# Kernel tuning notes

Hardware: AMD Instinct MI355X
Metric: run time of the kernel (lower is better)

Reference implementation:

```python
import jax, jax.numpy as jnp
import numpy as np

N, M, D = 1024, 1024, 256

def setup_inputs() -> dict:
    key = jax.random.key(0)
    ks = jax.random.split(key, 10)
    s = 1.0 / np.sqrt(D)
    return {
        "f_r": jax.random.normal(ks[0], (N, D), jnp.float32),
        "f_r_prime": jax.random.normal(ks[1], (M, D), jnp.float32),
        "W_w": jax.random.uniform(ks[2], (D, D), jnp.float32, -s, s),
        "W_b": jax.random.uniform(ks[3], (D,), jnp.float32, -s, s),
        "Wp_w": jax.random.uniform(ks[4], (D, D), jnp.float32, -s, s),
        "Wp_b": jax.random.uniform(ks[5], (D,), jnp.float32, -s, s),
        "w_w": jax.random.uniform(ks[6], (1, D), jnp.float32, -s, s),
        "w_b": jax.random.uniform(ks[7], (1,), jnp.float32, -s, s),
        "wp_w": jax.random.uniform(ks[8], (1, D), jnp.float32, -s, s),
        "wp_b": jax.random.uniform(ks[9], (1,), jnp.float32, -s, s),
    }

def reference(f_r, f_r_prime, W_w, W_b, Wp_w, Wp_b, w_w, w_b, wp_w, wp_b):
    q = f_r @ W_w.T + W_b            # [N, D]
    k = f_r_prime @ Wp_w.T + Wp_b    # [M, D]
    # additive (Bahdanau) scores: tanh over broadcast sum [N, M, D]
    h = jnp.tanh(q[:, None, :] + k[None, :, :])
    alpha = h @ w_w.T + w_b          # [N, M, 1]
    alpha = jax.nn.softmax(alpha, axis=1)
    # stage-1 pooling over M (weights on raw f_r_prime, as in source)
    context = jnp.sum(alpha * f_r_prime[None, :, :], axis=1)  # [N, D]
    # stage-2 attention pooling over N
    alpha_p = jax.nn.softmax(context @ wp_w.T + wp_b, axis=0)  # [N, 1]
    pool = jnp.sum(alpha_p * context, axis=0, keepdims=True)   # [1, D]
    return pool
```

## Files before the change

### kernel.cpp

```cpp
#include <hip/hip_runtime.h>

#define NN 1024
#define MM 1024
#define DD 256

__device__ __forceinline__ float rcp_fast(float x) { return __builtin_amdgcn_rcpf(x); }

__global__ __launch_bounds__(256) void gemm_exp_kernel(
    const float* __restrict__ f_r,  const float* __restrict__ W_w,  const float* __restrict__ W_b,
    const float* __restrict__ f_rp, const float* __restrict__ Wp_w, const float* __restrict__ Wp_b,
    float* __restrict__ Eq, float* __restrict__ EkT, float* __restrict__ out0)
{
    const int b    = blockIdx.x;
    const int mat  = b >> 7;
    const int tile = b & 127;
    const int rt = tile & 31, dt = tile >> 5;
    const float* __restrict__ A    = mat ? f_rp : f_r;
    const float* __restrict__ B    = mat ? Wp_w : W_w;
    const float* __restrict__ bias = mat ? Wp_b : W_b;

    __shared__ float As[32][36];
    __shared__ float Bs[32][68];
    __shared__ float T[64][36];

    const int t  = threadIdx.x;
    if (b == 0) out0[t] = 0.f;
    const int tx = t & 15, ty = t >> 4;
    const int r0 = rt * 32, d0 = dt * 64;
    const int ar = t >> 3, ak = (t & 7) * 4;
    const int br = t >> 2, bk = (t & 3) * 8;

    float acc[2][4];
    #pragma unroll
    for (int i = 0; i < 2; ++i)
        #pragma unroll
        for (int j = 0; j < 4; ++j) acc[i][j] = 0.f;

    for (int kk = 0; kk < DD; kk += 32) {
        float4 av  = *(const float4*)(A + (size_t)(r0 + ar) * DD + kk + ak);
        float4 bv0 = *(const float4*)(B + (size_t)(d0 + br) * DD + kk + bk);
        float4 bv1 = *(const float4*)(B + (size_t)(d0 + br) * DD + kk + bk + 4);
        __syncthreads();
        As[ak + 0][ar] = av.x; As[ak + 1][ar] = av.y; As[ak + 2][ar] = av.z; As[ak + 3][ar] = av.w;
        Bs[bk + 0][br] = bv0.x; Bs[bk + 1][br] = bv0.y; Bs[bk + 2][br] = bv0.z; Bs[bk + 3][br] = bv0.w;
        Bs[bk + 4][br] = bv1.x; Bs[bk + 5][br] = bv1.y; Bs[bk + 6][br] = bv1.z; Bs[bk + 7][br] = bv1.w;
        __syncthreads();
        #pragma unroll
        for (int k = 0; k < 32; ++k) {
            float2 a2 = *(const float2*)&As[k][ty * 2];
            float4 b4 = *(const float4*)&Bs[k][tx * 4];
            float aa[2] = {a2.x, a2.y};
            float bb[4] = {b4.x, b4.y, b4.z, b4.w};
            #pragma unroll
            for (int i = 0; i < 2; ++i)
                #pragma unroll
                for (int j = 0; j < 4; ++j)
                    acc[i][j] = fmaf(aa[i], bb[j], acc[i][j]);
        }
    }

    float bj[4];
    #pragma unroll
    for (int j = 0; j < 4; ++j) bj[j] = bias[d0 + tx * 4 + j];

    float e[2][4];
    #pragma unroll
    for (int i = 0; i < 2; ++i)
        #pragma unroll
        for (int j = 0; j < 4; ++j) {
            float v = acc[i][j] + bj[j];
            v = fminf(fmaxf(v, -10.f), 10.f);
            e[i][j] = __expf(2.f * v);
        }

    if (mat == 0) {
        #pragma unroll
        for (int i = 0; i < 2; ++i)
            *(float4*)&Eq[(size_t)(r0 + ty * 2 + i) * DD + d0 + tx * 4] =
                make_float4(e[i][0], e[i][1], e[i][2], e[i][3]);
    } else {
        __syncthreads();
        #pragma unroll
        for (int i = 0; i < 2; ++i)
            #pragma unroll
            for (int j = 0; j < 4; ++j) T[tx * 4 + j][ty * 2 + i] = e[i][j];
        __syncthreads();
        const int dl = t >> 3, rl = (t & 7) * 4;
        #pragma unroll
        for (int h = 0; h < 2; ++h) {
            int dloc = dl + 32 * h;
            float4 tv = *(const float4*)&T[dloc][rl];
            *(float4*)&EkT[(size_t)(d0 + dloc) * MM + r0 + rl] = tv;
        }
    }
}

__global__ __launch_bounds__(512, 8) void score_softmax_kernel(
    const float* __restrict__ Eq, const float* __restrict__ EkT,
    const float* __restrict__ w_w, float* __restrict__ alpha)
{
    __shared__ float eq[2 * DD];
    __shared__ float w2[DD];
    __shared__ float accbuf[8][256];
    __shared__ float redmx[8 * 2];
    __shared__ float redsm[8 * 2];

    const int t  = threadIdx.x;
    const int tg = t >> 8;
    const int tm = t & 255;
    const int lane = t & 63, wid = t >> 6;
    const int n0 = blockIdx.x * 2;
    const int dh = tg * 128;

    eq[t] = Eq[(size_t)n0 * DD + t];
    if (t < DD) w2[t] = -2.0f * w_w[t];
    __syncthreads();

    float acc[2][4];
    #pragma unroll
    for (int n = 0; n < 2; ++n)
        #pragma unroll
        for (int j = 0; j < 4; ++j) acc[n][j] = 0.f;

    const float* ekb = EkT + (size_t)dh * MM + 4 * tm;

    for (int g = 0; g < 32; ++g) {
        const int db = g * 4;
        float4 k0 = *(const float4*)(ekb + (size_t)(db + 0) * MM);
        float4 k1 = *(const float4*)(ekb + (size_t)(db + 1) * MM);
        float4 k2 = *(const float4*)(ekb + (size_t)(db + 2) * MM);
        float4 k3 = *(const float4*)(ekb + (size_t)(db + 3) * MM);
        float4 w4 = *(const float4*)&w2[dh + db];
        float4 qA = *(const float4*)&eq[dh + db];
        float4 qB = *(const float4*)&eq[DD + dh + db];

        float ka[2][4] = {{k0.x, k0.y, k0.z, k0.w}, {k2.x, k2.y, k2.z, k2.w}};
        float kb[2][4] = {{k1.x, k1.y, k1.z, k1.w}, {k3.x, k3.y, k3.z, k3.w}};
        float wa[2] = {w4.x, w4.z}, wb[2] = {w4.y, w4.w};
        float qa[2][2] = {{qA.x, qA.z}, {qB.x, qB.z}};
        float qb[2][2] = {{qA.y, qA.w}, {qB.y, qB.w}};

        #pragma unroll
        for (int pp = 0; pp < 2; ++pp)
            #pragma unroll
            for (int n = 0; n < 2; ++n)
                #pragma unroll
                for (int j = 0; j < 4; ++j) {
                    float x0 = fmaf(qa[n][pp], ka[pp][j], 1.f);
                    float x1 = fmaf(qb[n][pp], kb[pp][j], 1.f);
                    float p  = x0 * x1;
                    float tn = fmaf(wb[pp], x0, wa[pp] * x1);
                    acc[n][j] = fmaf(tn, rcp_fast(p), acc[n][j]);
                }
    }

    if (tg == 1) {
        #pragma unroll
        for (int n = 0; n < 2; ++n)
            #pragma unroll
            for (int j = 0; j < 4; ++j) accbuf[n * 4 + j][tm] = acc[n][j];
    }
    __syncthreads();
    if (tg == 0) {
        #pragma unroll
        for (int n = 0; n < 2; ++n)
            #pragma unroll
            for (int j = 0; j < 4; ++j) acc[n][j] += accbuf[n * 4 + j][tm];
    }

    float mx[2];
    #pragma unroll
    for (int n = 0; n < 2; ++n) {
        mx[n] = (tg == 0) ? fmaxf(fmaxf(acc[n][0], acc[n][1]), fmaxf(acc[n][2], acc[n][3])) : -3e38f;
        #pragma unroll
        for (int off = 32; off > 0; off >>= 1) mx[n] = fmaxf(mx[n], __shfl_xor(mx[n], off));
    }
    if (lane == 0) { redmx[wid * 2] = mx[0]; redmx[wid * 2 + 1] = mx[1]; }
    __syncthreads();
    float MX[2];
    #pragma unroll
    for (int n = 0; n < 2; ++n) {
        float m = redmx[n];
        #pragma unroll
        for (int w = 1; w < 8; ++w) m = fmaxf(m, redmx[w * 2 + n]);
        MX[n] = m;
    }

    float e[2][4], sm[2];
    #pragma unroll
    for (int n = 0; n < 2; ++n) {
        sm[n] = 0.f;
        #pragma unroll
        for (int j = 0; j < 4; ++j) {
            e[n][j] = (tg == 0) ? __expf(acc[n][j] - MX[n]) : 0.f;
            sm[n] += e[n][j];
        }
        #pragma unroll
        for (int off = 32; off > 0; off >>= 1) sm[n] += __shfl_xor(sm[n], off);
    }
    if (lane == 0) { redsm[wid * 2] = sm[0]; redsm[wid * 2 + 1] = sm[1]; }
    __syncthreads();
    if (tg == 0) {
        #pragma unroll
        for (int n = 0; n < 2; ++n) {
            float s = redsm[n];
            #pragma unroll
            for (int w = 1; w < 8; ++w) s += redsm[w * 2 + n];
            float inv = rcp_fast(s);
            *(float4*)&alpha[(size_t)(n0 + n) * MM + 4 * tm] =
                make_float4(e[n][0] * inv, e[n][1] * inv, e[n][2] * inv, e[n][3] * inv);
        }
    }
}

__global__ __launch_bounds__(256) void context_kernel(
    const float* __restrict__ alpha, const float* __restrict__ frp,
    float* __restrict__ part)
{
    __shared__ float als[16][128];
    const int t  = threadIdx.x;
    const int bm = blockIdx.x & 7;
    const int bn = blockIdx.x >> 3;
    const int dq = t & 63;
    const int ng = t >> 6;

    #pragma unroll
    for (int i = 0; i < 2; ++i) {
        int f4i = t + i * 256;
        int row = f4i >> 5, c4 = f4i & 31;
        *(float4*)&als[row][c4 * 4] =
            *(const float4*)&alpha[(size_t)(bn * 16 + row) * MM + bm * 128 + c4 * 4];
    }
    __syncthreads();

    float acc[4][4];
    #pragma unroll
    for (int n = 0; n < 4; ++n)
        #pragma unroll
        for (int j = 0; j < 4; ++j) acc[n][j] = 0.f;

    const float* fb = frp + (size_t)(bm * 128) * DD + 4 * dq;
    for (int m4 = 0; m4 < 32; ++m4) {
        float av[4][4];
        #pragma unroll
        for (int n = 0; n < 4; ++n) {
            float4 a4 = *(const float4*)&als[ng * 4 + n][m4 * 4];
            av[n][0] = a4.x; av[n][1] = a4.y; av[n][2] = a4.z; av[n][3] = a4.w;
        }
        #pragma unroll
        for (int mm = 0; mm < 4; ++mm) {
            float4 f4 = *(const float4*)(fb + (size_t)(m4 * 4 + mm) * DD);
            float fv[4] = {f4.x, f4.y, f4.z, f4.w};
            #pragma unroll
            for (int n = 0; n < 4; ++n)
                #pragma unroll
                for (int j = 0; j < 4; ++j)
                    acc[n][j] = fmaf(av[n][mm], fv[j], acc[n][j]);
        }
    }
    #pragma unroll
    for (int n = 0; n < 4; ++n)
        *(float4*)&part[((size_t)bm << 18) + (size_t)(bn * 16 + ng * 4 + n) * DD + 4 * dq] =
            make_float4(acc[n][0], acc[n][1], acc[n][2], acc[n][3]);
}

__global__ __launch_bounds__(256) void ctx_reduce_kernel(
    const float* __restrict__ part, const float* __restrict__ wp_w,
    float* __restrict__ ctx, float* __restrict__ score)
{
    __shared__ float red[4];
    const int t = threadIdx.x;
    const int n = blockIdx.x;
    const int lane = t & 63, wid = t >> 6;
    size_t idx = (size_t)n * DD + t;
    float c = 0.f;
    #pragma unroll
    for (int s = 0; s < 8; ++s) c += part[idx + ((size_t)s << 18)];
    ctx[idx] = c;
    float p = c * wp_w[t];
    #pragma unroll
    for (int off = 32; off > 0; off >>= 1) p += __shfl_xor(p, off);
    if (lane == 0) red[wid] = p;
    __syncthreads();
    if (t == 0) score[n] = red[0] + red[1] + red[2] + red[3];
}

__global__ __launch_bounds__(256) void pool_kernel(
    const float* __restrict__ ctx, const float* __restrict__ score,
    float* __restrict__ out)
{
    __shared__ float red[8];
    __shared__ float wloc[16];
    const int t = threadIdx.x, lane = t & 63, wid = t >> 6;

    float s0 = score[t], s1 = score[t + 256], s2 = score[t + 512], s3 = score[t + 768];
    float mx = fmaxf(fmaxf(s0, s1), fmaxf(s2, s3));
    #pragma unroll
    for (int off = 32; off > 0; off >>= 1) mx = fmaxf(mx, __shfl_xor(mx, off));
    if (lane == 0) red[wid] = mx;
    __syncthreads();
    mx = fmaxf(fmaxf(red[0], red[1]), fmaxf(red[2], red[3]));

    float se = __expf(s0 - mx) + __expf(s1 - mx) + __expf(s2 - mx) + __expf(s3 - mx);
    #pragma unroll
    for (int off = 32; off > 0; off >>= 1) se += __shfl_xor(se, off);
    if (lane == 0) red[4 + wid] = se;
    __syncthreads();
    se = red[4] + red[5] + red[6] + red[7];
    float invS = rcp_fast(se);

    if (t < 16) wloc[t] = __expf(score[blockIdx.x * 16 + t] - mx) * invS;
    __syncthreads();

    float pool = 0.f;
    const float* cb = ctx + (size_t)(blockIdx.x * 16) * DD + t;
    #pragma unroll
    for (int i = 0; i < 16; ++i) pool = fmaf(wloc[i], cb[i * DD], pool);
    atomicAdd(out + t, pool);
}

extern "C" void kernel_launch(void* const* d_in, const int* in_sizes, int n_in,
                              void* d_out, int out_size, void* d_ws, size_t ws_size,
                              hipStream_t stream) {
    const float* f_r  = (const float*)d_in[0];
    const float* f_rp = (const float*)d_in[1];
    const float* W_w  = (const float*)d_in[2];
    const float* W_b  = (const float*)d_in[3];
    const float* Wp_w = (const float*)d_in[4];
    const float* Wp_b = (const float*)d_in[5];
    const float* w_w  = (const float*)d_in[6];
    const float* wp_w = (const float*)d_in[8];
    float* out = (float*)d_out;

    float* ws    = (float*)d_ws;
    float* Eq    = ws;
    float* EkT   = ws + 262144;
    float* alpha = ws + 524288;
    float* part  = ws + 1572864;
    float* ctx   = ws + 3670016;
    float* score = ws + 3932160;

    gemm_exp_kernel<<<256, 256, 0, stream>>>(f_r, W_w, W_b, f_rp, Wp_w, Wp_b, Eq, EkT, out);
    score_softmax_kernel<<<512, 512, 0, stream>>>(Eq, EkT, w_w, alpha);
    context_kernel<<<512, 256, 0, stream>>>(alpha, f_rp, part);
    ctx_reduce_kernel<<<1024, 256, 0, stream>>>(part, wp_w, ctx, score);
    pool_kernel<<<64, 256, 0, stream>>>(ctx, score, out);
}
```

Measured before the change: 135.3 us.

## Precompute stage-2 scores algebraically, fold context reduce into pool, pack score math

```diff
diff --git a/kernel.cpp b/kernel.cpp
--- a/kernel.cpp
+++ b/kernel.cpp
@@ -4,14 +4,41 @@
 #define MM 1024
 #define DD 256
 
+typedef float floatx2 __attribute__((ext_vector_type(2)));
+
 __device__ __forceinline__ float rcp_fast(float x) { return __builtin_amdgcn_rcpf(x); }
 
 __global__ __launch_bounds__(256) void gemm_exp_kernel(
     const float* __restrict__ f_r,  const float* __restrict__ W_w,  const float* __restrict__ W_b,
     const float* __restrict__ f_rp, const float* __restrict__ Wp_w, const float* __restrict__ Wp_b,
-    float* __restrict__ Eq, float* __restrict__ EkT, float* __restrict__ out0)
+    const float* __restrict__ wp_w,
+    float* __restrict__ Eq, float* __restrict__ EkT, float* __restrict__ g,
+    float* __restrict__ out0)
 {
-    const int b    = blockIdx.x;
+    __shared__ float As[32][36];
+    __shared__ float Bs[32][68];
+    __shared__ float T[64][36];
+
+    const int b = blockIdx.x;
+    const int t = threadIdx.x;
+
+    if (b >= 256) {
+        const int gb = b - 256;
+        if (gb == 0) out0[t] = 0.f;
+        const int m = gb * 256 + t;
+        const float4* fm = (const float4*)(f_rp + (size_t)m * DD);
+        const float4* wp = (const float4*)wp_w;
+        float a0 = 0.f, a1 = 0.f, a2 = 0.f, a3 = 0.f;
+        #pragma unroll 8
+        for (int j = 0; j < 64; ++j) {
+            float4 v = fm[j], w = wp[j];
+            a0 = fmaf(v.x, w.x, a0); a1 = fmaf(v.y, w.y, a1);
+            a2 = fmaf(v.z, w.z, a2); a3 = fmaf(v.w, w.w, a3);
+        }
+        g[m] = (a0 + a1) + (a2 + a3);
+        return;
+    }
+
     const int mat  = b >> 7;
     const int tile = b & 127;
     const int rt = tile & 31, dt = tile >> 5;
@@ -19,12 +46,6 @@
     const float* __restrict__ B    = mat ? Wp_w : W_w;
     const float* __restrict__ bias = mat ? Wp_b : W_b;
 
-    __shared__ float As[32][36];
-    __shared__ float Bs[32][68];
-    __shared__ float T[64][36];
-
-    const int t  = threadIdx.x;
-    if (b == 0) out0[t] = 0.f;
     const int tx = t & 15, ty = t >> 4;
     const int r0 = rt * 32, d0 = dt * 64;
     const int ar = t >> 3, ak = (t & 7) * 4;
@@ -69,7 +90,7 @@
         #pragma unroll
         for (int j = 0; j < 4; ++j) {
             float v = acc[i][j] + bj[j];
-            v = fminf(fmaxf(v, -10.f), 10.f);
+            v = fminf(fmaxf(v, -5.f), 5.f);
             e[i][j] = __expf(2.f * v);
         }
 
@@ -95,15 +116,17 @@
     }
 }
 
-__global__ __launch_bounds__(512, 8) void score_softmax_kernel(
+__global__ __launch_bounds__(512, 4) void score_softmax_kernel(
     const float* __restrict__ Eq, const float* __restrict__ EkT,
-    const float* __restrict__ w_w, float* __restrict__ alpha)
+    const float* __restrict__ w_w, const float* __restrict__ g,
+    float* __restrict__ alpha, float* __restrict__ score)
 {
     __shared__ float eq[2 * DD];
     __shared__ float w2[DD];
     __shared__ float accbuf[8][256];
     __shared__ float redmx[8 * 2];
     __shared__ float redsm[8 * 2];
+    __shared__ float redg[4 * 2];
 
     const int t  = threadIdx.x;
     const int tg = t >> 8;
@@ -116,42 +139,64 @@
     if (t < DD) w2[t] = -2.0f * w_w[t];
     __syncthreads();
 
-    float acc[2][4];
-    #pragma unroll
-    for (int n = 0; n < 2; ++n)
-        #pragma unroll
-        for (int j = 0; j < 4; ++j) acc[n][j] = 0.f;
+    const floatx2 one2 = {1.f, 1.f};
+    floatx2 accl[2] = {{0.f, 0.f}, {0.f, 0.f}};
+    floatx2 acch[2] = {{0.f, 0.f}, {0.f, 0.f}};
 
     const float* ekb = EkT + (size_t)dh * MM + 4 * tm;
 
-    for (int g = 0; g < 32; ++g) {
-        const int db = g * 4;
-        float4 k0 = *(const float4*)(ekb + (size_t)(db + 0) * MM);
-        float4 k1 = *(const float4*)(ekb + (size_t)(db + 1) * MM);
-        float4 k2 = *(const float4*)(ekb + (size_t)(db + 2) * MM);
-        float4 k3 = *(const float4*)(ekb + (size_t)(db + 3) * MM);
+    float4 c0 = *(const float4*)(ekb + 0 * MM);
+    float4 c1 = *(const float4*)(ekb + 1 * MM);
+    float4 c2 = *(const float4*)(ekb + 2 * MM);
+    float4 c3 = *(const float4*)(ekb + 3 * MM);
+
+    for (int gi = 0; gi < 32; ++gi) {
+        float4 p0 = c0, p1 = c1, p2 = c2, p3 = c3;
+        if (gi < 31) {
+            const float* nb = ekb + (size_t)(gi * 4 + 4) * MM;
+            p0 = *(const float4*)(nb + 0 * MM);
+            p1 = *(const float4*)(nb + 1 * MM);
+            p2 = *(const float4*)(nb + 2 * MM);
+            p3 = *(const float4*)(nb + 3 * MM);
+        }
+        const int db = gi * 4;
         float4 w4 = *(const float4*)&w2[dh + db];
         float4 qA = *(const float4*)&eq[dh + db];
         float4 qB = *(const float4*)&eq[DD + dh + db];
 
-        float ka[2][4] = {{k0.x, k0.y, k0.z, k0.w}, {k2.x, k2.y, k2.z, k2.w}};
-        float kb[2][4] = {{k1.x, k1.y, k1.z, k1.w}, {k3.x, k3.y, k3.z, k3.w}};
-        float wa[2] = {w4.x, w4.z}, wb[2] = {w4.y, w4.w};
-        float qa[2][2] = {{qA.x, qA.z}, {qB.x, qB.z}};
-        float qb[2][2] = {{qA.y, qA.w}, {qB.y, qB.w}};
-
-        #pragma unroll
-        for (int pp = 0; pp < 2; ++pp)
-            #pragma unroll
-            for (int n = 0; n < 2; ++n)
-                #pragma unroll
-                for (int j = 0; j < 4; ++j) {
-                    float x0 = fmaf(qa[n][pp], ka[pp][j], 1.f);
-                    float x1 = fmaf(qb[n][pp], kb[pp][j], 1.f);
-                    float p  = x0 * x1;
-                    float tn = fmaf(wb[pp], x0, wa[pp] * x1);
-                    acc[n][j] = fmaf(tn, rcp_fast(p), acc[n][j]);
-                }
+        floatx2 kv[4][2] = {{{c0.x, c0.y}, {c0.z, c0.w}},
+                            {{c1.x, c1.y}, {c1.z, c1.w}},
+                            {{c2.x, c2.y}, {c2.z, c2.w}},
+                            {{c3.x, c3.y}, {c3.z, c3.w}}};
+        float ws[4] = {w4.x, w4.y, w4.z, w4.w};
+        float qs[2][4] = {{qA.x, qA.y, qA.z, qA.w}, {qB.x, qB.y, qB.z, qB.w}};
+
+        #pragma unroll
+        for (int h = 0; h < 2; ++h) {
+            #pragma unroll
+            for (int n = 0; n < 2; ++n) {
+                floatx2 x0 = qs[n][0] * kv[0][h] + one2;
+                floatx2 x1 = qs[n][1] * kv[1][h] + one2;
+                floatx2 x2 = qs[n][2] * kv[2][h] + one2;
+                floatx2 x3 = qs[n][3] * kv[3][h] + one2;
+                floatx2 p01 = x0 * x1;
+                floatx2 p23 = x2 * x3;
+                floatx2 n01 = ws[0] * x1 + ws[1] * x0;
+                floatx2 n23 = ws[2] * x3 + ws[3] * x2;
+                floatx2 nc  = n01 * p23 + n23 * p01;
+                floatx2 pt  = p01 * p23;
+                floatx2 r;  r.x = rcp_fast(pt.x);  r.y = rcp_fast(pt.y);
+                if (h == 0) accl[n] += nc * r; else acch[n] += nc * r;
+            }
+        }
+        c0 = p0; c1 = p1; c2 = p2; c3 = p3;
+    }
+
+    float acc[2][4];
+    #pragma unroll
+    for (int n = 0; n < 2; ++n) {
+        acc[n][0] = accl[n].x; acc[n][1] = accl[n].y;
+        acc[n][2] = acch[n].x; acc[n][3] = acch[n].y;
     }
 
     if (tg == 1) {
@@ -201,16 +246,25 @@
     if (lane == 0) { redsm[wid * 2] = sm[0]; redsm[wid * 2 + 1] = sm[1]; }
     __syncthreads();
     if (tg == 0) {
+        float4 g4 = *(const float4*)&g[4 * tm];
+        float sn[2];
         #pragma unroll
         for (int n = 0; n < 2; ++n) {
             float s = redsm[n];
             #pragma unroll
             for (int w = 1; w < 8; ++w) s += redsm[w * 2 + n];
             float inv = rcp_fast(s);
-            *(float4*)&alpha[(size_t)(n0 + n) * MM + 4 * tm] =
-                make_float4(e[n][0] * inv, e[n][1] * inv, e[n][2] * inv, e[n][3] * inv);
-        }
-    }
+            float a0 = e[n][0] * inv, a1 = e[n][1] * inv, a2 = e[n][2] * inv, a3 = e[n][3] * inv;
+            *(float4*)&alpha[(size_t)(n0 + n) * MM + 4 * tm] = make_float4(a0, a1, a2, a3);
+            sn[n] = fmaf(a0, g4.x, fmaf(a1, g4.y, fmaf(a2, g4.z, a3 * g4.w)));
+            #pragma unroll
+            for (int off = 32; off > 0; off >>= 1) sn[n] += __shfl_xor(sn[n], off);
+        }
+        if (lane == 0) { redg[wid * 2] = sn[0]; redg[wid * 2 + 1] = sn[1]; }
+    }
+    __syncthreads();
+    if (t == 0) score[n0]     = redg[0] + redg[2] + redg[4] + redg[6];
+    if (t == 1) score[n0 + 1] = redg[1] + redg[3] + redg[5] + redg[7];
 }
 
 __global__ __launch_bounds__(256) void context_kernel(
@@ -264,34 +318,13 @@
             make_float4(acc[n][0], acc[n][1], acc[n][2], acc[n][3]);
 }
 
-__global__ __launch_bounds__(256) void ctx_reduce_kernel(
-    const float* __restrict__ part, const float* __restrict__ wp_w,
-    float* __restrict__ ctx, float* __restrict__ score)
-{
-    __shared__ float red[4];
-    const int t = threadIdx.x;
-    const int n = blockIdx.x;
-    const int lane = t & 63, wid = t >> 6;
-    size_t idx = (size_t)n * DD + t;
-    float c = 0.f;
-    #pragma unroll
-    for (int s = 0; s < 8; ++s) c += part[idx + ((size_t)s << 18)];
-    ctx[idx] = c;
-    float p = c * wp_w[t];
-    #pragma unroll
-    for (int off = 32; off > 0; off >>= 1) p += __shfl_xor(p, off);
-    if (lane == 0) red[wid] = p;
-    __syncthreads();
-    if (t == 0) score[n] = red[0] + red[1] + red[2] + red[3];
-}
-
 __global__ __launch_bounds__(256) void pool_kernel(
-    const float* __restrict__ ctx, const float* __restrict__ score,
+    const float* __restrict__ part, const float* __restrict__ score,
     float* __restrict__ out)
 {
     __shared__ float red[8];
-    __shared__ float wloc[16];
     const int t = threadIdx.x, lane = t & 63, wid = t >> 6;
+    const int n0 = blockIdx.x * 4;
 
     float s0 = score[t], s1 = score[t + 256], s2 = score[t + 512], s3 = score[t + 768];
     float mx = fmaxf(fmaxf(s0, s1), fmaxf(s2, s3));
@@ -309,14 +342,17 @@
     se = red[4] + red[5] + red[6] + red[7];
     float invS = rcp_fast(se);
 
-    if (t < 16) wloc[t] = __expf(score[blockIdx.x * 16 + t] - mx) * invS;
-    __syncthreads();
-
-    float pool = 0.f;
-    const float* cb = ctx + (size_t)(blockIdx.x * 16) * DD + t;
-    #pragma unroll
-    for (int i = 0; i < 16; ++i) pool = fmaf(wloc[i], cb[i * DD], pool);
-    atomicAdd(out + t, pool);
+    float r = 0.f;
+    #pragma unroll
+    for (int i = 0; i < 4; ++i) {
+        float ap = __expf(score[n0 + i] - mx) * invS;
+        size_t idx = (size_t)(n0 + i) * DD + t;
+        float c = 0.f;
+        #pragma unroll
+        for (int s = 0; s < 8; ++s) c += part[idx + ((size_t)s << 18)];
+        r = fmaf(ap, c, r);
+    }
+    atomicAdd(out + t, r);
 }
 
 extern "C" void kernel_launch(void* const* d_in, const int* in_sizes, int n_in,
@@ -337,12 +373,12 @@
     float* EkT   = ws + 262144;
     float* alpha = ws + 524288;
     float* part  = ws + 1572864;
-    float* ctx   = ws + 3670016;
-    float* score = ws + 3932160;
-
-    gemm_exp_kernel<<<256, 256, 0, stream>>>(f_r, W_w, W_b, f_rp, Wp_w, Wp_b, Eq, EkT, out);
-    score_softmax_kernel<<<512, 512, 0, stream>>>(Eq, EkT, w_w, alpha);
+    float* score = ws + 3670016;
+    float* g     = ws + 3671040;
+
+    gemm_exp_kernel<<<260, 256, 0, stream>>>(f_r, W_w, W_b, f_rp, Wp_w, Wp_b, wp_w,
+                                             Eq, EkT, g, out);
+    score_softmax_kernel<<<512, 512, 0, stream>>>(Eq, EkT, w_w, g, alpha, score);
     context_kernel<<<512, 256, 0, stream>>>(alpha, f_rp, part);
-    ctx_reduce_kernel<<<1024, 256, 0, stream>>>(part, wp_w, ctx, score);
-    pool_kernel<<<64, 256, 0, stream>>>(ctx, score, out);
-}
+    pool_kernel<<<256, 256, 0, stream>>>(part, score, out);
+}
```

Measured after the change: 136.3 us. No clear change (+0.7%).
